# Kernel tuning notes

Measured on AMD Instinct MI355X. Metric: run time of the kernel, lower is better.

## Reference

```python
import jax, jax.numpy as jnp
import numpy as np

K = 11          # filterSize
EPS = 1e-3      # Charbonnier epsilon


def setup_inputs() -> dict:
    key = jax.random.key(0)
    k1, k2, k3 = jax.random.split(key, 3)
    N, C, H, W = 4, 3, 256, 256
    image1 = jax.random.normal(k1, (N, C, H, W), dtype=jnp.float32)
    image2 = jax.random.normal(k2, (N, C, H, W), dtype=jnp.float32)
    # per-pixel dynamic filters, shared across RGB channels
    filters = jax.random.uniform(k3, (N, K * K, H, W), dtype=jnp.float32)
    return {"image1": image1, "image2": image2, "filters": filters}


def _reconstruct(img, filters):
    # img: (N,C,H,W); filters: (N,K*K,H,W)
    N, C, H, W = img.shape
    pad = K // 2  # dilate=1, odd K -> symmetric zero pad
    p = jnp.pad(img, ((0, 0), (0, 0), (pad, pad), (pad, pad)))
    # Extract KxK patches in torch-unfold order (kh slow, kw fast):
    # (N, C, K*K, H, W)
    patches = jnp.stack(
        [p[:, :, i:i + H, j:j + W] for i in range(K) for j in range(K)],
        axis=2,
    )
    # per-pixel weighted sum over the K*K taps, filters broadcast over C
    return jnp.sum(patches * filters[:, None], axis=2)  # (N,C,H,W)


def reference(image1, image2, filters):
    recon = _reconstruct(image1, filters)
    diff = jnp.sqrt((recon - image2) ** 2 + EPS * EPS)  # Charbonnier
    return jnp.mean(diff)  # sum / (N*C*H*W)
```

## Files before the change

### kernel.cpp

```cpp
#include <hip/hip_runtime.h>
#include <math.h>

#define KF   11
#define PAD  5
#define NB   4
#define CH   3
#define HH   256
#define WW   256
#define HWSZ (HH * WW)
#define EPS2 (1e-3f * 1e-3f)

#define RPB   2
#define SROWS (RPB + KF - 1)
#define LW    272
#define LPAD  8
#define LW4   (LW / 4)
#define STOT  (CH * SROWS * LW4)

__global__ __launch_bounds__(256, 2) void recon_charbonnier_kernel(
    const float* __restrict__ image1,
    const float* __restrict__ image2,
    const float* __restrict__ filters,
    float* __restrict__ block_sums)
{
    __shared__ float limg[CH][SROWS][LW];
    __shared__ float part[CH][RPB][WW];
    __shared__ float wsum[4];

    const int tid  = threadIdx.x;
    const int p    = tid & 63;
    const int r    = (tid >> 6) & 1;
    const int half = tid >> 7;
    const int b    = blockIdx.x;
    const int n    = b >> 7;
    const int h0   = (b & 127) << 1;

    const float* __restrict__ img1n = image1 + (size_t)n * CH * HWSZ;

    for (int idx = tid; idx < STOT; idx += 256) {
        const int row = idx / LW4;
        const int c4  = idx - row * LW4;
        const int ch  = row / SROWS;
        const int rr  = row - ch * SROWS;
        const int grow = h0 + rr - PAD;
        const int gcol = (c4 << 2) - LPAD;
        float4 v = make_float4(0.f, 0.f, 0.f, 0.f);
        if ((unsigned)grow < (unsigned)HH && (unsigned)gcol <= (unsigned)(WW - 4))
            v = *(const float4*)(img1n + (size_t)ch * HWSZ
                                       + (size_t)grow * WW + gcol);
        *(float4*)&limg[ch][rr][c4 << 2] = v;
    }
    __syncthreads();

    const int w0 = p << 2;
    const float* __restrict__ fp = filters + (size_t)n * (KF * KF) * HWSZ
                                           + (size_t)(h0 + r) * WW + w0;

    const int dhBeg = half ? 6 : 0;
    const int dhCnt = half ? 5 : 6;

    float acc[CH][4] = {};
    float4 fv[KF], fvn[KF];

    #pragma unroll
    for (int dw = 0; dw < KF; ++dw)
        fv[dw] = *(const float4*)(fp + (size_t)(dhBeg * KF + dw) * HWSZ);

    for (int i = 0; i < dhCnt; ++i) {
        const int dh = dhBeg + i;
        if (i + 1 < dhCnt) {
            #pragma unroll
            for (int dw = 0; dw < KF; ++dw)
                fvn[dw] = *(const float4*)(fp + (size_t)((dh + 1) * KF + dw) * HWSZ);
        }

        #pragma unroll
        for (int ch = 0; ch < CH; ++ch) {
            const float* __restrict__ lrow = &limg[ch][r + dh][w0 + 3];
            float win[16];
            #pragma unroll
            for (int j = 0; j < 16; ++j) win[j] = lrow[j];

            #pragma unroll
            for (int dw = 0; dw < KF; ++dw) {
                acc[ch][0] = fmaf(fv[dw].x, win[dw + 0], acc[ch][0]);
                acc[ch][1] = fmaf(fv[dw].y, win[dw + 1], acc[ch][1]);
                acc[ch][2] = fmaf(fv[dw].z, win[dw + 2], acc[ch][2]);
                acc[ch][3] = fmaf(fv[dw].w, win[dw + 3], acc[ch][3]);
            }
        }

        #pragma unroll
        for (int dw = 0; dw < KF; ++dw) fv[dw] = fvn[dw];
    }

    if (half) {
        #pragma unroll
        for (int ch = 0; ch < CH; ++ch)
            *(float4*)&part[ch][r][w0] =
                make_float4(acc[ch][0], acc[ch][1], acc[ch][2], acc[ch][3]);
    }
    __syncthreads();

    float s = 0.f;
    if (!half) {
        const float* __restrict__ img2p = image2 + (size_t)n * CH * HWSZ
                                                 + (size_t)(h0 + r) * WW + w0;
        #pragma unroll
        for (int ch = 0; ch < CH; ++ch) {
            const float4 pr = *(const float4*)&part[ch][r][w0];
            const float4 t2 = *(const float4*)(img2p + (size_t)ch * HWSZ);
            const float d0 = acc[ch][0] + pr.x - t2.x;
            const float d1 = acc[ch][1] + pr.y - t2.y;
            const float d2 = acc[ch][2] + pr.z - t2.z;
            const float d3 = acc[ch][3] + pr.w - t2.w;
            s += sqrtf(d0 * d0 + EPS2) + sqrtf(d1 * d1 + EPS2)
               + sqrtf(d2 * d2 + EPS2) + sqrtf(d3 * d3 + EPS2);
        }
    }

    #pragma unroll
    for (int off = 32; off > 0; off >>= 1)
        s += __shfl_down(s, off, 64);
    if ((tid & 63) == 0) wsum[tid >> 6] = s;
    __syncthreads();
    if (tid == 0)
        block_sums[blockIdx.x] = (wsum[0] + wsum[1]) + (wsum[2] + wsum[3]);
}

__global__ __launch_bounds__(256) void final_reduce_kernel(
    const float* __restrict__ block_sums,
    float* __restrict__ out)
{
    float s = block_sums[threadIdx.x] + block_sums[threadIdx.x + 256];

    #pragma unroll
    for (int off = 32; off > 0; off >>= 1)
        s += __shfl_down(s, off, 64);

    __shared__ float wsum[4];
    if ((threadIdx.x & 63) == 0) wsum[threadIdx.x >> 6] = s;
    __syncthreads();
    if (threadIdx.x == 0) {
        const float inv_count = 1.0f / (float)(NB * CH * HH * WW);
        out[0] = ((wsum[0] + wsum[1]) + (wsum[2] + wsum[3])) * inv_count;
    }
}

extern "C" void kernel_launch(void* const* d_in, const int* in_sizes, int n_in,
                              void* d_out, int out_size, void* d_ws, size_t ws_size,
                              hipStream_t stream) {
    const float* image1  = (const float*)d_in[0];
    const float* image2  = (const float*)d_in[1];
    const float* filters = (const float*)d_in[2];
    float* out = (float*)d_out;
    float* block_sums = (float*)d_ws;

    const int grid = NB * (HH / RPB);

    recon_charbonnier_kernel<<<grid, 256, 0, stream>>>(image1, image2, filters,
                                                       block_sums);
    final_reduce_kernel<<<1, 256, 0, stream>>>(block_sums, out);
}
```

Before: 31.51 us.

## Prefetch filters and image2 before LDS barrier, ping-pong filter buffers, vectorize LDS reads

The first filter row and the image2 values are now loaded before the shared-memory tile fill and barrier, so their global latency overlaps the image tile load. The filter-row loop is unrolled by two with ping-pong register buffers, removing the per-iteration register copy of the prefetched filters. LDS window reads switch from scalar to aligned float4 loads over a 20-element window. The cost is more live registers (two 11-float4 filter buffers plus image2 values), which may strain the 2-blocks-per-CU launch bound.

```diff
diff --git a/kernel.cpp b/kernel.cpp
--- a/kernel.cpp
+++ b/kernel.cpp
@@ -37,6 +37,18 @@
 
     const float* __restrict__ img1n = image1 + (size_t)n * CH * HWSZ;
 
+    const int w0 = p << 2;
+    const float* __restrict__ fp = filters + (size_t)n * (KF * KF) * HWSZ
+                                           + (size_t)(h0 + r) * WW + w0;
+    const int dhBeg = half ? 6 : 0;
+    const int dhCnt = half ? 5 : 6;
+
+    float4 fvA[KF], fvB[KF];
+
+    #pragma unroll
+    for (int dw = 0; dw < KF; ++dw)
+        fvA[dw] = *(const float4*)(fp + (size_t)(dhBeg * KF + dw) * HWSZ);
+
     for (int idx = tid; idx < STOT; idx += 256) {
         const int row = idx / LW4;
         const int c4  = idx - row * LW4;
@@ -50,49 +62,61 @@
                                        + (size_t)grow * WW + gcol);
         *(float4*)&limg[ch][rr][c4 << 2] = v;
     }
+
+    const float* __restrict__ img2p = image2 + (size_t)n * CH * HWSZ
+                                             + (size_t)(h0 + r) * WW + w0;
+    float4 t2[CH];
+    if (!half) {
+        #pragma unroll
+        for (int ch = 0; ch < CH; ++ch)
+            t2[ch] = *(const float4*)(img2p + (size_t)ch * HWSZ);
+    }
+
     __syncthreads();
 
-    const int w0 = p << 2;
-    const float* __restrict__ fp = filters + (size_t)n * (KF * KF) * HWSZ
-                                           + (size_t)(h0 + r) * WW + w0;
+    float acc[CH][4] = {};
 
-    const int dhBeg = half ? 6 : 0;
-    const int dhCnt = half ? 5 : 6;
+    #define COMPUTE_DH(FV, dh)                                                 \
+        do {                                                                   \
+            _Pragma("unroll")                                                  \
+            for (int ch = 0; ch < CH; ++ch) {                                  \
+                float win[20];                                                 \
+                _Pragma("unroll")                                              \
+                for (int k = 0; k < 5; ++k) {                                  \
+                    const float4 q =                                           \
+                        *(const float4*)&limg[ch][r + (dh)][w0 + (k << 2)];    \
+                    win[4 * k + 0] = q.x;                                      \
+                    win[4 * k + 1] = q.y;                                      \
+                    win[4 * k + 2] = q.z;                                      \
+                    win[4 * k + 3] = q.w;                                      \
+                }                                                              \
+                _Pragma("unroll")                                              \
+                for (int dw = 0; dw < KF; ++dw) {                              \
+                    acc[ch][0] = fmaf(FV[dw].x, win[dw + 3], acc[ch][0]);      \
+                    acc[ch][1] = fmaf(FV[dw].y, win[dw + 4], acc[ch][1]);      \
+                    acc[ch][2] = fmaf(FV[dw].z, win[dw + 5], acc[ch][2]);      \
+                    acc[ch][3] = fmaf(FV[dw].w, win[dw + 6], acc[ch][3]);      \
+                }                                                              \
+            }                                                                  \
+        } while (0)
 
-    float acc[CH][4] = {};
-    float4 fv[KF], fvn[KF];
+    #define LOAD_DH(FV, dh)                                                    \
+        do {                                                                   \
+            _Pragma("unroll")                                                  \
+            for (int dw = 0; dw < KF; ++dw)                                    \
+                FV[dw] = *(const float4*)(fp + (size_t)((dh) * KF + dw) * HWSZ); \
+        } while (0)
 
-    #pragma unroll
-    for (int dw = 0; dw < KF; ++dw)
-        fv[dw] = *(const float4*)(fp + (size_t)(dhBeg * KF + dw) * HWSZ);
+    for (int i = 0; i < dhCnt; i += 2) {
+        const int dh = dhBeg + i;
+        if (i + 1 < dhCnt) LOAD_DH(fvB, dh + 1);
+        COMPUTE_DH(fvA, dh);
+        if (i + 2 < dhCnt) LOAD_DH(fvA, dh + 2);
+        if (i + 1 < dhCnt) COMPUTE_DH(fvB, dh + 1);
+    }
 
-    for (int i = 0; i < dhCnt; ++i) {
-        const int dh = dhBeg + i;
-        if (i + 1 < dhCnt) {
-            #pragma unroll
-            for (int dw = 0; dw < KF; ++dw)
-                fvn[dw] = *(const float4*)(fp + (size_t)((dh + 1) * KF + dw) * HWSZ);
-        }
-
-        #pragma unroll
-        for (int ch = 0; ch < CH; ++ch) {
-            const float* __restrict__ lrow = &limg[ch][r + dh][w0 + 3];
-            float win[16];
-            #pragma unroll
-            for (int j = 0; j < 16; ++j) win[j] = lrow[j];
-
-            #pragma unroll
-            for (int dw = 0; dw < KF; ++dw) {
-                acc[ch][0] = fmaf(fv[dw].x, win[dw + 0], acc[ch][0]);
-                acc[ch][1] = fmaf(fv[dw].y, win[dw + 1], acc[ch][1]);
-                acc[ch][2] = fmaf(fv[dw].z, win[dw + 2], acc[ch][2]);
-                acc[ch][3] = fmaf(fv[dw].w, win[dw + 3], acc[ch][3]);
-            }
-        }
-
-        #pragma unroll
-        for (int dw = 0; dw < KF; ++dw) fv[dw] = fvn[dw];
-    }
+    #undef COMPUTE_DH
+    #undef LOAD_DH
 
     if (half) {
         #pragma unroll
@@ -104,16 +128,13 @@
 
     float s = 0.f;
     if (!half) {
-        const float* __restrict__ img2p = image2 + (size_t)n * CH * HWSZ
-                                                 + (size_t)(h0 + r) * WW + w0;
         #pragma unroll
         for (int ch = 0; ch < CH; ++ch) {
             const float4 pr = *(const float4*)&part[ch][r][w0];
-            const float4 t2 = *(const float4*)(img2p + (size_t)ch * HWSZ);
-            const float d0 = acc[ch][0] + pr.x - t2.x;
-            const float d1 = acc[ch][1] + pr.y - t2.y;
-            const float d2 = acc[ch][2] + pr.z - t2.z;
-            const float d3 = acc[ch][3] + pr.w - t2.w;
+            const float d0 = acc[ch][0] + pr.x - t2[ch].x;
+            const float d1 = acc[ch][1] + pr.y - t2[ch].y;
+            const float d2 = acc[ch][2] + pr.z - t2[ch].z;
+            const float d3 = acc[ch][3] + pr.w - t2[ch].w;
             s += sqrtf(d0 * d0 + EPS2) + sqrtf(d1 * d1 + EPS2)
                + sqrtf(d2 * d2 + EPS2) + sqrtf(d3 * d3 + EPS2);
         }
```

Result: faster. 30.75 us (-2.4%).
